# Optimization experiments

Measured on AMD Instinct MI355X. Metric: run time of the kernel, lower is better.

Reference implementation:

```python
import jax, jax.numpy as jnp
import numpy as np

IN_C, OUT_C, K, STRIDE = 128, 256, 3, 1

def setup_inputs() -> dict:
    key = jax.random.key(0)
    k1, k2 = jax.random.split(key)
    x = jax.random.normal(k1, (32, IN_C, 112, 112), dtype=jnp.float32)
    weight = jax.random.normal(k2, (OUT_C, IN_C, K, K), dtype=jnp.float32)
    bias = jnp.zeros((OUT_C,), dtype=jnp.float32)
    return {"x": x, "weight": weight, "bias": bias}

def reference(x, weight, bias):
    # valid-padding direct conv, NCHW / OIHW layout, stride STRIDE
    out = jax.lax.conv_general_dilated(
        x, weight,
        window_strides=(STRIDE, STRIDE),
        padding='VALID',
        dimension_numbers=('NCHW', 'OIHW', 'NCHW'))
    return out + bias[None, :, None, None]
```

## Files before the change

kernel.cpp:

```cpp
#include <hip/hip_runtime.h>

#define NI 32
#define CI 128
#define HI 112
#define WI 112
#define OC 256
#define HO 110
#define WO 110

typedef float f32x4 __attribute__((ext_vector_type(4)));
typedef short s16x8 __attribute__((ext_vector_type(8)));

typedef const unsigned int __attribute__((address_space(1))) gu32;
typedef unsigned int __attribute__((address_space(3))) lu32;

__device__ __forceinline__ ushort f2bf(float f) {
  union { float f; unsigned int u; } x; x.f = f;
  unsigned int r = x.u + 0x7FFFu + ((x.u >> 16) & 1u);
  return (ushort)(r >> 16);
}

__global__ __launch_bounds__(256) void pack_w_kernel(const float* __restrict__ w,
                                                     ushort* __restrict__ wp) {
  int i = blockIdx.x * 256 + threadIdx.x;
  int e = i & 7;
  int k8 = (i >> 3) & 3;
  int oc = (i >> 5) & 255;
  int cc = (i >> 13) & 1;
  int chalf = (i >> 14) & 1;
  int kk = i >> 15;
  int ch = chalf * 64 + cc * 32 + k8 * 8 + e;
  int kh = kk / 3, kw = kk - kh * 3;
  wp[i] = f2bf(w[((oc * CI + ch) * 3 + kh) * 3 + kw]);
}

__global__ __launch_bounds__(256) void to_nhwc_kernel(const float* __restrict__ x,
                                                      ushort* __restrict__ xn) {
  __shared__ ushort lds[1792 * 8];
  int b = blockIdx.x;
  int n = b / HI;
  int h = b - n * HI;
  const float* xr = x + ((size_t)n * CI * HI) * WI + (size_t)h * WI;
  int t = threadIdx.x;
  int w = t & 127;
  int cph = t >> 7;
  if (w < WI) {
    #pragma unroll
    for (int it = 0; it < 32; ++it) {
      int cp = it * 2 + cph;
      int c = cp * 2;
      float f0 = xr[(size_t)c * (HI * WI) + w];
      float f1 = xr[(size_t)(c + 1) * (HI * WI) + w];
      unsigned int pk = (unsigned int)f2bf(f0) | ((unsigned int)f2bf(f1) << 16);
      int chunk = w * 16 + ((cp >> 2) ^ (w & 15));
      *(unsigned int*)((char*)lds + chunk * 16 + (cp & 3) * 4) = pk;
    }
  }
  __syncthreads();
  #pragma unroll
  for (int it = 0; it < 7; ++it) {
    int j = it * 256 + t;
    int w2 = j >> 4, c8 = j & 15;
    int src = w2 * 16 + (c8 ^ (w2 & 15));
    uint4 v = *(const uint4*)((const char*)lds + src * 16);
    int chalf = c8 >> 3, c8i = c8 & 7;
    *(uint4*)&xn[((((size_t)n * 2 + chalf) * HI + h) * WI + w2) * 64 + c8i * 8] = v;
  }
}

__global__ __launch_bounds__(256, 2) void conv_mfma_kernel(const ushort* __restrict__ xn,
                                                           const ushort* __restrict__ wp,
                                                           const float* __restrict__ bias,
                                                           float* __restrict__ out) {
  __shared__ ushort lds[340 * 64];
  const int bid = blockIdx.x;
  const int n = bid / HO;
  const int oh = bid - n * HO;
  const int t = threadIdx.x;
  const int lane = t & 63;
  const int wid = t >> 6;
  const int lane15 = lane & 15;
  const int laneh = lane >> 4;
  const int oc0 = wid * 64;
  char* ldsb = (char*)lds;

  f32x4 acc[4][7] = {};
  s16x8 abuf[2][4];

  #pragma unroll
  for (int chalf = 0; chalf < 2; ++chalf) {
    if (chalf) __syncthreads();
    const char* gsb = (const char*)(xn + (((size_t)n * 2 + chalf) * HI + oh) * (WI * 64));
    #pragma unroll
    for (int i = 0; i < 11; ++i) {
      int idx = i * 256 + t;
      if (idx < 2688) {
        int L = idx * 16;
        int go = L ^ (((L >> 7) & 7) << 4);
        __builtin_amdgcn_global_load_lds((gu32*)(gsb + go), (lu32*)(ldsb + L), 16, 0, 0);
      }
    }
    {
      const ushort* wb = wp + ((size_t)(chalf * 2)) * 8192 + (oc0 + lane15) * 32 + laneh * 8;
      #pragma unroll
      for (int mf = 0; mf < 4; ++mf) abuf[0][mf] = *(const s16x8*)(wb + mf * 512);
    }
    __syncthreads();

    #pragma unroll
    for (int sc = 0; sc < 18; ++sc) {
      const int kk = sc >> 1, cc = sc & 1;
      const int kh = kk / 3, kw = kk - kh * 3;
      if (sc < 17) {
        const int kk2 = (sc + 1) >> 1, cc2 = (sc + 1) & 1;
        const ushort* wb = wp + ((size_t)((kk2 * 2 + chalf) * 2 + cc2)) * 8192 +
                           (oc0 + lane15) * 32 + laneh * 8;
        #pragma unroll
        for (int mf = 0; mf < 4; ++mf) abuf[(sc + 1) & 1][mf] = *(const s16x8*)(wb + mf * 512);
      }
      s16x8 b[7];
      #pragma unroll
      for (int nf = 0; nf < 7; ++nf) {
        int R = kh * WI + nf * 16 + lane15 + kw;
        int addr = (R << 7) + (((laneh * 16) ^ ((R & 7) << 4)) ^ (cc << 6));
        b[nf] = *(const s16x8*)(ldsb + addr);
      }
      #pragma unroll
      for (int mf = 0; mf < 4; ++mf)
        #pragma unroll
        for (int nf = 0; nf < 7; ++nf)
          acc[mf][nf] = __builtin_amdgcn_mfma_f32_16x16x32_bf16(abuf[sc & 1][mf], b[nf],
                                                                acc[mf][nf], 0, 0, 0);
    }
  }

  float* outb = out + ((size_t)n * OC) * (HO * WO) + (size_t)oh * WO;
  #pragma unroll
  for (int mf = 0; mf < 4; ++mf) {
    #pragma unroll
    for (int r = 0; r < 4; ++r) {
      const int oc = oc0 + mf * 16 + laneh * 4 + r;
      const float bv = bias[oc];
      float* op = outb + (size_t)oc * (HO * WO);
      #pragma unroll
      for (int nf = 0; nf < 7; ++nf) {
        int ow = nf * 16 + lane15;
        if (ow < WO) op[ow] = acc[mf][nf][r] + bv;
      }
    }
  }
}

__global__ __launch_bounds__(256) void conv_naive_kernel(const float* __restrict__ x,
                                                         const float* __restrict__ w,
                                                         const float* __restrict__ bias,
                                                         float* __restrict__ out) {
  long i = (long)blockIdx.x * 256 + threadIdx.x;
  const long total = (long)NI * OC * HO * WO;
  if (i >= total) return;
  int ow = (int)(i % WO);
  long r1 = i / WO;
  int oh = (int)(r1 % HO);
  long r2 = r1 / HO;
  int oc = (int)(r2 % OC);
  int n = (int)(r2 / OC);
  float s = bias[oc];
  const float* xb = x + ((size_t)n * CI * HI) * WI;
  const float* wb = w + (size_t)oc * CI * 9;
  for (int c = 0; c < CI; ++c)
    for (int kh = 0; kh < 3; ++kh)
      for (int kw = 0; kw < 3; ++kw)
        s += xb[((size_t)c * HI + oh + kh) * WI + ow + kw] * wb[(c * 3 + kh) * 3 + kw];
  out[i] = s;
}

extern "C" void kernel_launch(void* const* d_in, const int* in_sizes, int n_in,
                              void* d_out, int out_size, void* d_ws, size_t ws_size,
                              hipStream_t stream) {
  const float* x = (const float*)d_in[0];
  const float* w = (const float*)d_in[1];
  const float* bias = (const float*)d_in[2];
  float* out = (float*)d_out;

  const size_t xn_elems = (size_t)NI * 2 * HI * WI * 64;
  const size_t wp_elems = (size_t)9 * 2 * 2 * 256 * 32;
  const size_t need = (xn_elems + wp_elems) * sizeof(ushort);

  if (ws_size >= need) {
    ushort* xnw = (ushort*)d_ws;
    ushort* wpw = xnw + xn_elems;
    hipLaunchKernelGGL(pack_w_kernel, dim3((unsigned)(wp_elems / 256)), dim3(256), 0, stream,
                       w, wpw);
    hipLaunchKernelGGL(to_nhwc_kernel, dim3(NI * HI), dim3(256), 0, stream, x, xnw);
    hipLaunchKernelGGL(conv_mfma_kernel, dim3(NI * HO), dim3(256), 0, stream, xnw, wpw, bias,
                       out);
  } else {
    long total = (long)NI * OC * HO * WO;
    hipLaunchKernelGGL(conv_naive_kernel, dim3((unsigned)((total + 255) / 256)), dim3(256), 0,
                       stream, x, w, bias, out);
  }
}
```

Before: 372.1 us.

## Double-buffer input channel quarters in LDS and remap block order

Splits input channels into four 32-channel quarters, changing both the NHWC staging layout and the weight packing to match. The conv kernel now keeps two LDS buffers, so the next quarter's global-to-LDS load is issued while MFMAs run on the current one. This is meant to hide the load latency that previously stalled every channel half. It also permutes block indices across eight groups, likely to spread work across XCDs for cache locality, and raises wave priority around the MFMA burst. LDS use per block stays about the same, but there are now more syncs and a new swizzle pattern.

After: 299.9 us. 1.24x faster.

```diff
diff --git a/kernel.cpp b/kernel.cpp
--- a/kernel.cpp
+++ b/kernel.cpp
@@ -26,10 +26,9 @@
   int e = i & 7;
   int k8 = (i >> 3) & 3;
   int oc = (i >> 5) & 255;
-  int cc = (i >> 13) & 1;
-  int chalf = (i >> 14) & 1;
+  int cq = (i >> 13) & 3;
   int kk = i >> 15;
-  int ch = chalf * 64 + cc * 32 + k8 * 8 + e;
+  int ch = cq * 32 + k8 * 8 + e;
   int kh = kk / 3, kw = kk - kh * 3;
   wp[i] = f2bf(w[((oc * CI + ch) * 3 + kh) * 3 + kw]);
 }
@@ -63,8 +62,8 @@
     int w2 = j >> 4, c8 = j & 15;
     int src = w2 * 16 + (c8 ^ (w2 & 15));
     uint4 v = *(const uint4*)((const char*)lds + src * 16);
-    int chalf = c8 >> 3, c8i = c8 & 7;
-    *(uint4*)&xn[((((size_t)n * 2 + chalf) * HI + h) * WI + w2) * 64 + c8i * 8] = v;
+    int cq = c8 >> 2, g = c8 & 3;
+    *(uint4*)&xn[((((size_t)n * 4 + cq) * HI + h) * WI + w2) * 32 + g * 8] = v;
   }
 }
 
@@ -72,10 +71,11 @@
                                                            const ushort* __restrict__ wp,
                                                            const float* __restrict__ bias,
                                                            float* __restrict__ out) {
-  __shared__ ushort lds[340 * 64];
+  __shared__ ushort lds[2 * 340 * 32];
   const int bid = blockIdx.x;
-  const int n = bid / HO;
-  const int oh = bid - n * HO;
+  const int orig = (bid & 7) * 440 + (bid >> 3);
+  const int n = orig / HO;
+  const int oh = orig - n * HO;
   const int t = threadIdx.x;
   const int lane = t & 63;
   const int wid = t >> 6;
@@ -87,50 +87,69 @@
   f32x4 acc[4][7] = {};
   s16x8 abuf[2][4];
 
+  {
+    const char* gsb = (const char*)(xn + ((((size_t)n * 4 + 0) * HI + oh) * WI) * 32);
+    #pragma unroll
+    for (int i = 0; i < 6; ++i) {
+      int idx = i * 256 + t;
+      if (idx < 1344) {
+        int L = idx * 16;
+        int go = L ^ (((L >> 7) & 3) << 4);
+        __builtin_amdgcn_global_load_lds((gu32*)(gsb + go), (lu32*)(ldsb + L), 16, 0, 0);
+      }
+    }
+    const ushort* wb = wp + (oc0 + lane15) * 32 + laneh * 8;
+    #pragma unroll
+    for (int mf = 0; mf < 4; ++mf) abuf[0][mf] = *(const s16x8*)(wb + mf * 512);
+  }
+  __syncthreads();
+
   #pragma unroll
-  for (int chalf = 0; chalf < 2; ++chalf) {
-    if (chalf) __syncthreads();
-    const char* gsb = (const char*)(xn + (((size_t)n * 2 + chalf) * HI + oh) * (WI * 64));
-    #pragma unroll
-    for (int i = 0; i < 11; ++i) {
-      int idx = i * 256 + t;
-      if (idx < 2688) {
-        int L = idx * 16;
-        int go = L ^ (((L >> 7) & 7) << 4);
-        __builtin_amdgcn_global_load_lds((gu32*)(gsb + go), (lu32*)(ldsb + L), 16, 0, 0);
-      }
-    }
-    {
-      const ushort* wb = wp + ((size_t)(chalf * 2)) * 8192 + (oc0 + lane15) * 32 + laneh * 8;
-      #pragma unroll
-      for (int mf = 0; mf < 4; ++mf) abuf[0][mf] = *(const s16x8*)(wb + mf * 512);
-    }
-    __syncthreads();
-
-    #pragma unroll
-    for (int sc = 0; sc < 18; ++sc) {
-      const int kk = sc >> 1, cc = sc & 1;
+  for (int q = 0; q < 4; ++q) {
+    if (q) __syncthreads();
+    const int qb = (q & 1) * 21760;
+    #pragma unroll
+    for (int kk = 0; kk < 9; ++kk) {
+      const int g = q * 9 + kk;
       const int kh = kk / 3, kw = kk - kh * 3;
-      if (sc < 17) {
-        const int kk2 = (sc + 1) >> 1, cc2 = (sc + 1) & 1;
-        const ushort* wb = wp + ((size_t)((kk2 * 2 + chalf) * 2 + cc2)) * 8192 +
-                           (oc0 + lane15) * 32 + laneh * 8;
+      if (g + 1 < 36) {
+        const int g2 = g + 1;
+        const int q2 = g2 / 9, kk2 = g2 - q2 * 9;
+        const ushort* wb = wp + ((size_t)(kk2 * 4 + q2)) * 8192 + (oc0 + lane15) * 32 +
+                           laneh * 8;
         #pragma unroll
-        for (int mf = 0; mf < 4; ++mf) abuf[(sc + 1) & 1][mf] = *(const s16x8*)(wb + mf * 512);
+        for (int mf = 0; mf < 4; ++mf)
+          abuf[g2 & 1][mf] = *(const s16x8*)(wb + mf * 512);
+      }
+      if (kk == 0 && q < 3) {
+        const char* gsb =
+            (const char*)(xn + ((((size_t)n * 4 + (q + 1)) * HI + oh) * WI) * 32);
+        char* ldst = ldsb + (((q + 1) & 1) * 21760);
+        #pragma unroll
+        for (int i = 0; i < 6; ++i) {
+          int idx = i * 256 + t;
+          if (idx < 1344) {
+            int L = idx * 16;
+            int go = L ^ (((L >> 7) & 3) << 4);
+            __builtin_amdgcn_global_load_lds((gu32*)(gsb + go), (lu32*)(ldst + L), 16, 0, 0);
+          }
+        }
       }
       s16x8 b[7];
       #pragma unroll
       for (int nf = 0; nf < 7; ++nf) {
         int R = kh * WI + nf * 16 + lane15 + kw;
-        int addr = (R << 7) + (((laneh * 16) ^ ((R & 7) << 4)) ^ (cc << 6));
+        int addr = qb + (R << 6) + ((laneh ^ ((R >> 1) & 3)) << 4);
         b[nf] = *(const s16x8*)(ldsb + addr);
       }
+      __builtin_amdgcn_s_setprio(1);
       #pragma unroll
       for (int mf = 0; mf < 4; ++mf)
         #pragma unroll
         for (int nf = 0; nf < 7; ++nf)
-          acc[mf][nf] = __builtin_amdgcn_mfma_f32_16x16x32_bf16(abuf[sc & 1][mf], b[nf],
+          acc[mf][nf] = __builtin_amdgcn_mfma_f32_16x16x32_bf16(abuf[g & 1][mf], b[nf],
                                                                 acc[mf][nf], 0, 0, 0);
+      __builtin_amdgcn_s_setprio(0);
     }
   }
 
@@ -182,8 +201,8 @@
   const float* bias = (const float*)d_in[2];
   float* out = (float*)d_out;
 
-  const size_t xn_elems = (size_t)NI * 2 * HI * WI * 64;
-  const size_t wp_elems = (size_t)9 * 2 * 2 * 256 * 32;
+  const size_t xn_elems = (size_t)NI * 4 * HI * WI * 32;
+  const size_t wp_elems = (size_t)9 * 4 * 256 * 32;
   const size_t need = (xn_elems + wp_elems) * sizeof(ushort);
 
   if (ws_size >= need) {
```
